# Kernel tuning notes

Hardware: AMD Instinct MI355X
Metric: run time of the kernel (lower is better)

The kernel has to match this reference:

```python
import jax, jax.numpy as jnp
import numpy as np
import math

B, N_TOK, C, H = 8, 1024, 384, 6
K, S, P = 3, 2, 1
OUT_C, HID = 384, 4 * 384
EPS = 1e-5
NEG_INF = float('-inf')


def _build_conv_mask(num_token, k, s, p):
    """Replicates ConvAttentionMask (include_cls_token=True). Returns (mask[(N+2),(N+2)], idx[(W,k^2)] with -1 for padding)."""
    I = int(math.sqrt(num_token))
    ref = np.arange(num_token).reshape(I, I)
    ref = np.pad(ref, ((0, p), (0, p)), constant_values=-1)
    cent = np.arange(k // 2 - p, I - k // 2 + p, s)
    cc = np.stack(np.meshgrid(cent, cent, indexing='ij'), -1).reshape(-1, 1, 2)  # cartesian_prod order
    ke = np.arange(-(k // 2), k // 2 + 1)
    kc = np.stack(np.meshgrid(ke, ke, indexing='ij'), -1).reshape(1, -1, 2)
    coords = cc + kc  # (W, k^2, 2); negative coords wrap like torch fancy indexing -> hit -1 padding
    idx = ref[coords[..., 0], coords[..., 1]]  # (W, k^2)
    mask = np.full((num_token, num_token), NEG_INF, np.float32)
    for w in idx:
        v = w[w >= 0]
        mask[np.ix_(v, v)] = 1.0
    idx = idx + (idx >= 0).astype(np.int32)  # shift for cls token; -1 stays -1
    mask = np.pad(mask, ((1, 0), (1, 0)), constant_values=1.0)  # cls row/col
    mask = np.pad(mask, ((0, 1), (0, 1)), constant_values=0.0)  # extra zero-padded token
    return mask, idx

MASK_NP, IDX_NP = _build_conv_mask(N_TOK, K, S, P)
W_WIN = IDX_NP.shape[0]
# torch negative index -1 on a length-(N_TOK+1) tensor -> wrap to last token
IDX_FLAT = np.where(IDX_NP < 0, IDX_NP + N_TOK + 1, IDX_NP).reshape(-1)


def _ln(x, w, b):
    mu = jnp.mean(x, -1, keepdims=True)
    var = jnp.mean(jnp.square(x - mu), -1, keepdims=True)
    return (x - mu) * jax.lax.rsqrt(var + EPS) * w + b


def setup_inputs() -> dict:
    key = jax.random.key(0)
    ks = jax.random.split(key, 8)
    sd = 0.02
    return {
        'x': jax.random.normal(ks[0], (B, N_TOK + 1, C), jnp.float32),
        'norm1_w': jnp.ones((C,), jnp.float32), 'norm1_b': jnp.zeros((C,), jnp.float32),
        'qkv_w': sd * jax.random.normal(ks[1], (3 * C, C), jnp.float32),
        'proj_w': sd * jax.random.normal(ks[2], (C, C), jnp.float32),
        'proj_b': jnp.zeros((C,), jnp.float32),
        'norm2_w': jnp.ones((C,), jnp.float32), 'norm2_b': jnp.zeros((C,), jnp.float32),
        'pool_w': sd * jax.random.normal(ks[3], (C, K * K * C), jnp.float32),
        'pool_b': jnp.zeros((C,), jnp.float32),
        'norm3_w': jnp.ones((C,), jnp.float32), 'norm3_b': jnp.zeros((C,), jnp.float32),
        'fc1_w': sd * jax.random.normal(ks[4], (HID, C), jnp.float32),
        'fc1_b': jnp.zeros((HID,), jnp.float32),
        'fc2_w': sd * jax.random.normal(ks[5], (OUT_C, HID), jnp.float32),
        'fc2_b': jnp.zeros((OUT_C,), jnp.float32),
    }


def reference(x, norm1_w, norm1_b, qkv_w, proj_w, proj_b, norm2_w, norm2_b,
              pool_w, pool_b, norm3_w, norm3_b, fc1_w, fc1_b, fc2_w, fc2_b):
    mask = jnp.asarray(MASK_NP)  # (N_TOK+2, N_TOK+2), values in {-inf, 0, 1}
    Bv, N, Cv = x.shape
    d = Cv // H
    h = _ln(x, norm1_w, norm1_b)
    h = jnp.pad(h, ((0, 0), (0, 1), (0, 0)))  # append zero token -> (B, N+1, C)
    M = N + 1
    # attention (scale = num_heads**-0.5 as in the source, qkv has no bias)
    qkv = (h @ qkv_w.T).reshape(Bv, M, 3, H, d).transpose(2, 0, 3, 1, 4)
    q, k, v = qkv[0], qkv[1], qkv[2]
    scores = jnp.einsum('bhqd,bhkd->bhqk', q, k) * (H ** -0.5)
    # multiplicative mask {-inf,0,1}: keep where 1, zero where 0, -inf where -inf (intended semantics)
    scores = jnp.where(mask == 1.0, scores, jnp.where(mask == 0.0, 0.0, NEG_INF))
    probs = jax.nn.softmax(scores, axis=-1)
    attn = jnp.einsum('bhqk,bhkd->bhqd', probs, v).transpose(0, 2, 1, 3).reshape(Bv, M, Cv)
    attn = attn @ proj_w.T + proj_b
    h = h + attn
    h = h[:, :-1, :]  # drop padded token -> (B, N, C)
    h = _ln(h, norm2_w, norm2_b)
    # conv-style pooling: gather k^2 tokens per window, project
    gathered = h[:, IDX_FLAT, :].reshape(Bv, W_WIN, K * K * Cv)
    tok = gathered @ pool_w.T + pool_b  # (B, W, C)
    h = jnp.concatenate([h[:, :1, :], tok], axis=1)  # prepend cls -> (B, W+1, C)
    h = _ln(h, norm3_w, norm3_b)
    h = jax.nn.gelu(h @ fc1_w.T + fc1_b, approximate=False)
    return h @ fc2_w.T + fc2_b  # (B, W+1, OUT_C)
```

## Files before the change

### kernel.cpp

```cpp
#include <hip/hip_runtime.h>


typedef unsigned short u16;
typedef unsigned int u32;
typedef short s16x8 __attribute__((ext_vector_type(8)));
typedef float f32x4 __attribute__((ext_vector_type(4)));

__device__ __forceinline__ float b2f(u16 u) {
    return __uint_as_float(((u32)u) << 16);
}
__device__ __forceinline__ u16 f2b(float f) {
    u32 u = __float_as_uint(f);
    return (u16)((u + 0x7FFFu + ((u >> 16) & 1u)) >> 16);
}
__device__ __forceinline__ void gload16(const void* g, void* l) {
    __builtin_amdgcn_global_load_lds(
        (const __attribute__((address_space(1))) void*)g,
        (__attribute__((address_space(3))) void*)l, 16, 0, 0);
}
__device__ __forceinline__ float wave_sum(float v) {
#pragma unroll
    for (int o = 32; o > 0; o >>= 1) v += __shfl_xor(v, o, 64);
    return v;
}
__device__ __forceinline__ float wave_max(float v) {
#pragma unroll
    for (int o = 32; o > 0; o >>= 1) v = fmaxf(v, __shfl_xor(v, o, 64));
    return v;
}
__device__ __forceinline__ float half_sum(float v) {
#pragma unroll
    for (int o = 16; o > 0; o >>= 1) v += __shfl_xor(v, o, 64);
    return v;
}
__device__ __forceinline__ float half_max(float v) {
#pragma unroll
    for (int o = 16; o > 0; o >>= 1) v = fmaxf(v, __shfl_xor(v, o, 64));
    return v;
}
__device__ __forceinline__ float dot8(const float* qsh, int d0, uint4 u) {
    return qsh[d0 + 0] * b2f((u16)(u.x)) + qsh[d0 + 1] * b2f((u16)(u.x >> 16)) +
           qsh[d0 + 2] * b2f((u16)(u.y)) + qsh[d0 + 3] * b2f((u16)(u.y >> 16)) +
           qsh[d0 + 4] * b2f((u16)(u.z)) + qsh[d0 + 5] * b2f((u16)(u.z >> 16)) +
           qsh[d0 + 6] * b2f((u16)(u.w)) + qsh[d0 + 7] * b2f((u16)(u.w >> 16));
}

#define CCH 384
#define SCALE 0.40824829046386302f
#define NEG_BIG (-1e30f)

#define W_QKV 0
#define W_PROJ 442368
#define W_POOL 589824
#define W_FC1 1916928
#define W_FC2 2506752
#define W_TOTAL 3096576

__device__ __forceinline__ void ln_from_f32(const float* in, const float* w,
                                            const float* bb, u16* out,
                                            int lane) {
    float v[6];
    float s = 0.f, ss = 0.f;
#pragma unroll
    for (int i = 0; i < 6; i++) {
        v[i] = in[lane + 64 * i];
        s += v[i];
        ss += v[i] * v[i];
    }
    s = wave_sum(s);
    ss = wave_sum(ss);
    float mu = s * (1.f / 384.f);
    float var = ss * (1.f / 384.f) - mu * mu;
    float inv = rsqrtf(var + 1e-5f);
#pragma unroll
    for (int i = 0; i < 6; i++) {
        int c = lane + 64 * i;
        out[c] = f2b((v[i] - mu) * inv * w[c] + bb[c]);
    }
}
__device__ __forceinline__ void ln_from_b16(const u16* in, const float* w,
                                            const float* bb, u16* out,
                                            int lane) {
    float v[6];
    float s = 0.f, ss = 0.f;
#pragma unroll
    for (int i = 0; i < 6; i++) {
        v[i] = b2f(in[lane + 64 * i]);
        s += v[i];
        ss += v[i] * v[i];
    }
    s = wave_sum(s);
    ss = wave_sum(ss);
    float mu = s * (1.f / 384.f);
    float var = ss * (1.f / 384.f) - mu * mu;
    float inv = rsqrtf(var + 1e-5f);
#pragma unroll
    for (int i = 0; i < 6; i++) {
        int c = lane + 64 * i;
        out[c] = f2b((v[i] - mu) * inv * w[c] + bb[c]);
    }
}

#define PRO_LN 2052
#define PRO_CVT 1512
#define PRO_ZERO 771
__global__ __launch_bounds__(256) void prologue(
    const float* __restrict__ x, const float* __restrict__ n1w,
    const float* __restrict__ n1b, u16* __restrict__ h1,
    const float* __restrict__ qkv_w, const float* __restrict__ proj_w,
    const float* __restrict__ pool_w, const float* __restrict__ fc1_w,
    const float* __restrict__ fc2_w, u16* __restrict__ wb,
    float* __restrict__ dout) {
    int bid = blockIdx.x, tid = threadIdx.x;
    if (bid < PRO_LN) {
        int wv = tid >> 6, lane = tid & 63;
        int row = bid * 4 + wv;
        int t = row % 1026, b = row / 1026;
        u16* out = h1 + (size_t)row * CCH;
        if (t == 1025) {
#pragma unroll
            for (int i = 0; i < 6; i++) out[lane + 64 * i] = 0;
            return;
        }
        ln_from_f32(x + ((size_t)b * 1025 + t) * CCH, n1w, n1b, out, lane);
    } else if (bid < PRO_LN + PRO_CVT) {
        size_t off = ((size_t)(bid - PRO_LN) * 256 + tid) * 8;
        if (off >= W_TOTAL) return;
        const float* src;
        size_t base;
        if (off < W_PROJ)       { src = qkv_w;  base = W_QKV; }
        else if (off < W_POOL)  { src = proj_w; base = W_PROJ; }
        else if (off < W_FC1)   { src = pool_w; base = W_POOL; }
        else if (off < W_FC2)   { src = fc1_w;  base = W_FC1; }
        else                    { src = fc2_w;  base = W_FC2; }
        size_t rel = off - base;
        float4 a = *(const float4*)(src + rel);
        float4 b = *(const float4*)(src + rel + 4);
        uint4 o;
        o.x = (u32)f2b(a.x) | ((u32)f2b(a.y) << 16);
        o.y = (u32)f2b(a.z) | ((u32)f2b(a.w) << 16);
        o.z = (u32)f2b(b.x) | ((u32)f2b(b.y) << 16);
        o.w = (u32)f2b(b.z) | ((u32)f2b(b.w) << 16);
        *(uint4*)(wb + off) = o;
    } else {
        size_t idx = ((size_t)(bid - PRO_LN - PRO_CVT) * 256 + tid) * 4;
        *(float4*)(dout + idx) = make_float4(0.f, 0.f, 0.f, 0.f);
    }
}

#define MID_LN 2050
#define MID_ZERO 768
__global__ __launch_bounds__(256) void midk(u16* __restrict__ h,
                                            const float* __restrict__ n2w,
                                            const float* __restrict__ n2b,
                                            float* __restrict__ tokf) {
    int bid = blockIdx.x, tid = threadIdx.x;
    if (bid < MID_LN) {
        int wv = tid >> 6, lane = tid & 63;
        int row = bid * 4 + wv;
        int b = row / 1025, t = row % 1025;
        u16* p = h + ((size_t)b * 1026 + t) * CCH;
        ln_from_b16(p, n2w, n2b, p, lane);
    } else {
        size_t idx = ((size_t)(bid - MID_LN) * 256 + tid) * 4;
        *(float4*)(tokf + idx) = make_float4(0.f, 0.f, 0.f, 0.f);
    }
}

__global__ __launch_bounds__(256) void ln3_concat(const u16* __restrict__ h2,
                                                  const float* __restrict__ tokf,
                                                  const float* __restrict__ w,
                                                  const float* __restrict__ bb,
                                                  u16* __restrict__ h3) {
    int tid = threadIdx.x;
    int wv = tid >> 6, lane = tid & 63;
    int row = blockIdx.x * 4 + wv;
    int b = row / 257, t = row % 257;
    u16* out = h3 + (size_t)row * CCH;
    if (t == 0) {
        ln_from_b16(h2 + (size_t)b * 1026 * CCH, w, bb, out, lane);
    } else {
        ln_from_f32(tokf + ((size_t)b * 256 + (t - 1)) * CCH, w, bb, out, lane);
    }
}

template <int TN, bool GATHER, int SPLITK, bool BIAS, bool GELU_ACT, bool RES,
          bool ATOMIC>
__global__ __launch_bounds__(256) void gemm_mf(const u16* __restrict__ A,
                                               int lda,
                                               const u16* __restrict__ Bwb,
                                               const float* __restrict__ bias,
                                               const u16* __restrict__ Res,
                                               void* __restrict__ Yv, int M,
                                               int N, int K) {
    __shared__ u16 Asl[128 * 32];
    __shared__ u16 Bsl[TN * 32];
    const int tid = threadIdx.x;
    const int wave = tid >> 6, lane = tid & 63;
    const int quad = lane >> 4, l15 = lane & 15;
    const int wvu = __builtin_amdgcn_readfirstlane(wave);
    const int m0 = blockIdx.y * 128, n0 = blockIdx.x * TN;
    const int kp = (SPLITK > 1) ? blockIdx.z : 0;
    const int KS = K / SPLITK;
    const int kbase = kp * KS;
    const int srow = tid >> 2;
    const int sseg = (tid & 3) ^ (srow & 3);

    f32x4 acc[2][TN / 16];
#pragma unroll
    for (int i = 0; i < 2; i++)
#pragma unroll
        for (int j = 0; j < TN / 16; j++) acc[i][j] = (f32x4){0.f, 0.f, 0.f, 0.f};

    for (int kt = 0; kt < KS; kt += 32) {
        const int kk = kbase + kt;
        const int kf = kk + sseg * 8;
#pragma unroll
        for (int L = 0; L < 2; L++) {
            int row = L * 64 + srow;
            const u16* src;
            if (GATHER) {
                int m = m0 + row;
                int b = m >> 8, w = m & 255;
                int j = kf / 384, rem = kf - j * 384;
                int pr = 2 * (w >> 4) + j / 3 - 1;
                int pc = 2 * (w & 15) + j % 3 - 1;
                int tok = (pr >= 0 && pr < 32 && pc >= 0 && pc < 32)
                              ? (32 * pr + pc + 1)
                              : 1024;
                src = A + ((size_t)b * 1026 + tok) * 384 + rem;
            } else {
                int m = m0 + row;
                if (m >= M) m = M - 1;
                src = A + (size_t)m * lda + kf;
            }
            gload16(src, &Asl[(size_t)(L * 256 + wvu * 64) * 8]);
        }
#pragma unroll
        for (int L = 0; L < TN / 64; L++) {
            int row = L * 64 + srow;
            gload16(Bwb + (size_t)(n0 + row) * K + kf,
                    &Bsl[(size_t)(L * 256 + wvu * 64) * 8]);
        }
        __syncthreads();
        s16x8 afr[2], bfr[TN / 16];
        const int rslot = (quad ^ (l15 & 3)) * 8;
#pragma unroll
        for (int ms = 0; ms < 2; ms++)
            afr[ms] =
                *(const s16x8*)(&Asl[(wave * 32 + ms * 16 + l15) * 32 + rslot]);
#pragma unroll
        for (int ns = 0; ns < TN / 16; ns++)
            bfr[ns] = *(const s16x8*)(&Bsl[(ns * 16 + l15) * 32 + rslot]);
#pragma unroll
        for (int ms = 0; ms < 2; ms++)
#pragma unroll
            for (int ns = 0; ns < TN / 16; ns++)
                acc[ms][ns] = __builtin_amdgcn_mfma_f32_16x16x32_bf16(
                    afr[ms], bfr[ns], acc[ms][ns], 0, 0, 0);
        __syncthreads();
    }
#pragma unroll
    for (int ms = 0; ms < 2; ms++) {
#pragma unroll
        for (int ns = 0; ns < TN / 16; ns++) {
            int n = n0 + ns * 16 + l15;
#pragma unroll
            for (int i = 0; i < 4; i++) {
                int m = m0 + wave * 32 + ms * 16 + quad * 4 + i;
                if (m >= M) continue;
                float v = acc[ms][ns][i];
                if (BIAS && (SPLITK == 1 || kp == 0)) v += bias[n];
                if (RES) v += b2f(Res[(size_t)m * N + n]);
                if (GELU_ACT) v = 0.5f * v * (1.f + erff(v * 0.70710678118f));
                if (ATOMIC)
                    atomicAdd((float*)Yv + (size_t)m * N + n, v);
                else
                    ((u16*)Yv)[(size_t)m * N + n] = f2b(v);
            }
        }
    }
}

__global__ __launch_bounds__(256) void attn_patch(u16* __restrict__ qkv) {
    __shared__ float qsh[4][2][64];
    int tid = threadIdx.x;
    int wv = tid >> 6, lane = tid & 63;
    int pair = blockIdx.x * 4 + wv;
    int idx = pair & 511;
    int hb = pair >> 9;
    int h = hb % 6, b = hb / 6;
    int hl = lane >> 5, l5 = lane & 31;
    int p0 = idx * 2;
    int p = p0 | hl;
    int r = p >> 5, c = p & 31;
    int rlo, rhi, clo, chi;
    if (r & 1) { rlo = (r - 2 < 0) ? 0 : r - 2; rhi = (r + 2 > 31) ? 31 : r + 2; }
    else       { rlo = (r - 1 < 0) ? 0 : r - 1; rhi = (r + 1 > 31) ? 31 : r + 1; }
    if (c & 1) { clo = (c - 2 < 0) ? 0 : c - 2; chi = (c + 2 > 31) ? 31 : c + 2; }
    else       { clo = (c - 1 < 0) ? 0 : c - 1; chi = (c + 1 > 31) ? 31 : c + 1; }
    int nr = rhi - rlo + 1, nc = chi - clo + 1;
    int nk = nr * nc + 1;
    int tok = 0;
    if (l5 >= 1 && l5 < nk) {
        int jj = l5 - 1;
        tok = 1 + ((rlo + jj / nc) << 5) + (clo + jj % nc);
    }
    u16* base = qkv + (size_t)b * 1026 * 1152 + h * 64;
    qsh[wv][0][lane] = b2f(base[(size_t)(1 + p0) * 1152 + lane]);
    qsh[wv][1][lane] = b2f(base[(size_t)(2 + p0) * 1152 + lane]);
    float sc = NEG_BIG;
    if (l5 < nk) {
        const u16* krow = base + (size_t)tok * 1152 + 384;
        float acc = 0.f;
#pragma unroll
        for (int d0 = 0; d0 < 64; d0 += 8)
            acc += dot8(qsh[wv][hl], d0, *(const uint4*)(krow + d0));
        sc = acc * SCALE;
    }
    float mx = fmaxf(half_max(sc), 0.f);
    float pe = (l5 < nk) ? expf(sc - mx) : 0.f;
    float Z = half_sum(pe) + expf(-mx);
    float o0 = 0.f, o1 = 0.f;
#pragma unroll
    for (int j = 0; j < 26; j++) {
        int t = __shfl(tok, (hl << 5) | j, 64);
        float wj = __shfl(pe, (hl << 5) | j, 64);
        u32 vv = *(const u32*)(base + (size_t)t * 1152 + 768 + 2 * l5);
        o0 += wj * b2f((u16)vv);
        o1 += wj * b2f((u16)(vv >> 16));
    }
    float zi = 1.f / Z;
    u32 packed = (u32)f2b(o0 * zi) | ((u32)f2b(o1 * zi) << 16);
    *(u32*)(base + (size_t)(1 + p) * 1152 + 2 * l5) = packed;
}

__global__ __launch_bounds__(1024) void attn_cls(u16* __restrict__ qkv) {
    int h = blockIdx.x % 6, b = blockIdx.x / 6;
    u16* base = qkv + (size_t)b * 1026 * 1152 + h * 64;
    int tid = threadIdx.x, lane = tid & 63, wv = tid >> 6;
    __shared__ float sc[1026];
    __shared__ float qsh[64];
    __shared__ float redmax[16], redsum[16];
    __shared__ float pv[16][64];
    if (tid < 64) qsh[tid] = b2f(base[tid]);
    __syncthreads();
    for (int key = tid; key < 1026; key += 1024) {
        const u16* krow = base + (size_t)key * 1152 + 384;
        float acc = 0.f;
#pragma unroll
        for (int d0 = 0; d0 < 64; d0 += 8)
            acc += dot8(qsh, d0, *(const uint4*)(krow + d0));
        sc[key] = acc * SCALE;
    }
    __syncthreads();
    float lm = NEG_BIG;
    for (int key = tid; key < 1026; key += 1024) lm = fmaxf(lm, sc[key]);
    lm = wave_max(lm);
    if (lane == 0) redmax[wv] = lm;
    __syncthreads();
    float mx = NEG_BIG;
#pragma unroll
    for (int i = 0; i < 16; i++) mx = fmaxf(mx, redmax[i]);
    float lsum = 0.f;
    for (int key = tid; key < 1026; key += 1024) {
        float e = expf(sc[key] - mx);
        sc[key] = e;
        lsum += e;
    }
    lsum = wave_sum(lsum);
    if (lane == 0) redsum[wv] = lsum;
    __syncthreads();
    float Z = 0.f;
#pragma unroll
    for (int i = 0; i < 16; i++) Z += redsum[i];
    float acc = 0.f;
#pragma unroll
    for (int t = 0; t < 65; t++) {
        int key = wv + 16 * t;
        bool ok = key < 1026;
        int kc = ok ? key : 1025;
        float p = ok ? sc[kc] : 0.f;
        acc += p * b2f(base[(size_t)kc * 1152 + 768 + lane]);
    }
    pv[wv][lane] = acc;
    __syncthreads();
    if (tid < 64) {
        float s = 0.f;
#pragma unroll
        for (int w2 = 0; w2 < 16; w2++) s += pv[w2][tid];
        base[tid] = f2b(s / Z);
        base[(size_t)1025 * 1152 + tid] = 0;
    }
}

extern "C" void kernel_launch(void* const* d_in, const int* in_sizes, int n_in,
                              void* d_out, int out_size, void* d_ws,
                              size_t ws_size, hipStream_t stream) {
    const float* x      = (const float*)d_in[0];
    const float* n1w    = (const float*)d_in[1];
    const float* n1b    = (const float*)d_in[2];
    const float* qkv_w  = (const float*)d_in[3];
    const float* proj_w = (const float*)d_in[4];
    const float* proj_b = (const float*)d_in[5];
    const float* n2w    = (const float*)d_in[6];
    const float* n2b    = (const float*)d_in[7];
    const float* pool_w = (const float*)d_in[8];
    const float* pool_b = (const float*)d_in[9];
    const float* n3w    = (const float*)d_in[10];
    const float* n3b    = (const float*)d_in[11];
    const float* fc1_w  = (const float*)d_in[12];
    const float* fc1_b  = (const float*)d_in[13];
    const float* fc2_w  = (const float*)d_in[14];
    const float* fc2_b  = (const float*)d_in[15];

    u16* ws = (u16*)d_ws;
    u16* h1    = ws;
    u16* qkvb  = ws + 3151872;
    u16* wb    = ws + 12607488;
    float* tokf = (float*)qkvb;
    u16* h3    = qkvb + 1572864;
    u16* mlp1  = qkvb + 2362368;

    prologue<<<PRO_LN + PRO_CVT + PRO_ZERO, 256, 0, stream>>>(
        x, n1w, n1b, h1, qkv_w, proj_w, pool_w, fc1_w, fc2_w, wb,
        (float*)d_out);
    gemm_mf<128, false, 1, false, false, false, false>
        <<<dim3(1152 / 128, 65), 256, 0, stream>>>(h1, 384, wb + W_QKV,
                                                   nullptr, nullptr, qkvb,
                                                   8208, 1152, 384);
    attn_patch<<<8 * 6 * 512 / 4, 256, 0, stream>>>(qkvb);
    attn_cls<<<8 * 6, 1024, 0, stream>>>(qkvb);
    gemm_mf<64, false, 1, true, false, true, false>
        <<<dim3(384 / 64, 65), 256, 0, stream>>>(qkvb, 1152, wb + W_PROJ,
                                                 proj_b, h1, h1, 8208, 384,
                                                 384);
    midk<<<MID_LN + MID_ZERO, 256, 0, stream>>>(h1, n2w, n2b, tokf);
    gemm_mf<64, true, 4, true, false, false, true>
        <<<dim3(384 / 64, 16, 4), 256, 0, stream>>>(h1, 384, wb + W_POOL,
                                                    pool_b, nullptr, tokf,
                                                    2048, 384, 3456);
    ln3_concat<<<8 * 257 / 4, 256, 0, stream>>>(h1, tokf, n3w, n3b, h3);
    gemm_mf<64, false, 1, true, true, false, false>
        <<<dim3(1536 / 64, 17), 256, 0, stream>>>(h3, 384, wb + W_FC1, fc1_b,
                                                  nullptr, mlp1, 2056, 1536,
                                                  384);
    gemm_mf<64, false, 4, true, false, false, true>
        <<<dim3(384 / 64, 17, 4), 256, 0, stream>>>(mlp1, 1536, wb + W_FC2,
                                                    fc2_b, nullptr, d_out,
                                                    2056, 384, 1536);
}
```

Measured before the change: 265.5 us.

## Stage shared K/V window tile in LDS for patch attention blocks

Each block of four query pairs (eight adjacent patch tokens in one row) now cooperatively loads the union of their 5x11 neighbourhood K and V rows, plus the cls token, into swizzled LDS using direct global-to-LDS loads. The score and PV loops then read from LDS instead of issuing scattered global loads per lane. This removes redundant global reads of overlapping neighbours across queries, at the cost of 16KB LDS per block and a block-wide barrier. Out-of-range slots point at the padding token.

Result: no change. 269.8 us (+1.6%).

```diff
diff --git a/kernel.cpp b/kernel.cpp
--- a/kernel.cpp
+++ b/kernel.cpp
@@ -283,17 +283,50 @@
 }
 
 __global__ __launch_bounds__(256) void attn_patch(u16* __restrict__ qkv) {
+    __shared__ u16 Ksh[64 * 64];
+    __shared__ u16 Vsh[64 * 64];
     __shared__ float qsh[4][2][64];
     int tid = threadIdx.x;
     int wv = tid >> 6, lane = tid & 63;
-    int pair = blockIdx.x * 4 + wv;
-    int idx = pair & 511;
-    int hb = pair >> 9;
+    int pair0 = blockIdx.x * 4;
+    int idx0 = pair0 & 511;
+    int hb = pair0 >> 9;
     int h = hb % 6, b = hb / 6;
+    int r = idx0 >> 4;
+    int c0 = (idx0 & 15) * 2;
+    u16* base = qkv + (size_t)b * 1026 * 1152 + h * 64;
+
+    int p0 = (idx0 + wv) * 2;
+    qsh[wv][0][lane] = b2f(base[(size_t)(1 + p0) * 1152 + lane]);
+    qsh[wv][1][lane] = b2f(base[(size_t)(2 + p0) * 1152 + lane]);
+
+#pragma unroll
+    for (int i = 0; i < 4; i++) {
+        int chunk = wv * 4 + i;
+        int isV = chunk >> 3;
+        int slot = (chunk & 7) * 8 + (lane >> 3);
+        int seg = lane & 7;
+        int tok;
+        if (slot < 55) {
+            int sr = slot / 11, sc2 = slot - sr * 11;
+            int kr = r - 2 + sr, kc = c0 - 1 + sc2;
+            tok = (kr >= 0 && kr < 32 && kc >= 0 && kc < 32)
+                      ? (1 + (kr << 5) + kc)
+                      : 1025;
+        } else {
+            tok = (slot == 55) ? 0 : 1025;
+        }
+        int sseg = seg ^ (slot & 7);
+        const u16* src =
+            base + (size_t)tok * 1152 + (isV ? 768 : 384) + sseg * 8;
+        u16* dst = (isV ? Vsh : Ksh) + (size_t)(chunk & 7) * 512;
+        gload16(src, dst);
+    }
+    __syncthreads();
+
     int hl = lane >> 5, l5 = lane & 31;
-    int p0 = idx * 2;
     int p = p0 | hl;
-    int r = p >> 5, c = p & 31;
+    int c = p & 31;
     int rlo, rhi, clo, chi;
     if (r & 1) { rlo = (r - 2 < 0) ? 0 : r - 2; rhi = (r + 2 > 31) ? 31 : r + 2; }
     else       { rlo = (r - 1 < 0) ? 0 : r - 1; rhi = (r + 1 > 31) ? 31 : r + 1; }
@@ -301,21 +334,22 @@
     else       { clo = (c - 1 < 0) ? 0 : c - 1; chi = (c + 1 > 31) ? 31 : c + 1; }
     int nr = rhi - rlo + 1, nc = chi - clo + 1;
     int nk = nr * nc + 1;
-    int tok = 0;
-    if (l5 >= 1 && l5 < nk) {
+    int slot = 56;
+    if (l5 == 0) slot = 55;
+    else if (l5 < nk) {
         int jj = l5 - 1;
-        tok = 1 + ((rlo + jj / nc) << 5) + (clo + jj % nc);
-    }
-    u16* base = qkv + (size_t)b * 1026 * 1152 + h * 64;
-    qsh[wv][0][lane] = b2f(base[(size_t)(1 + p0) * 1152 + lane]);
-    qsh[wv][1][lane] = b2f(base[(size_t)(2 + p0) * 1152 + lane]);
+        int kr = rlo + jj / nc, kc = clo + jj % nc;
+        slot = (kr - (r - 2)) * 11 + (kc - (c0 - 1));
+    }
     float sc = NEG_BIG;
     if (l5 < nk) {
-        const u16* krow = base + (size_t)tok * 1152 + 384;
+        const u16* krow = Ksh + slot * 64;
+        int sw = slot & 7;
         float acc = 0.f;
 #pragma unroll
-        for (int d0 = 0; d0 < 64; d0 += 8)
-            acc += dot8(qsh[wv][hl], d0, *(const uint4*)(krow + d0));
+        for (int d0 = 0; d0 < 8; d0++)
+            acc += dot8(qsh[wv][hl], d0 * 8,
+                        *(const uint4*)(krow + (d0 ^ sw) * 8));
         sc = acc * SCALE;
     }
     float mx = fmaxf(half_max(sc), 0.f);
@@ -324,9 +358,11 @@
     float o0 = 0.f, o1 = 0.f;
 #pragma unroll
     for (int j = 0; j < 26; j++) {
-        int t = __shfl(tok, (hl << 5) | j, 64);
+        int ts = __shfl(slot, (hl << 5) | j, 64);
         float wj = __shfl(pe, (hl << 5) | j, 64);
-        u32 vv = *(const u32*)(base + (size_t)t * 1152 + 768 + 2 * l5);
+        const u16* vrow = Vsh + ts * 64;
+        int g = (l5 >> 2) ^ (ts & 7);
+        u32 vv = *(const u32*)(vrow + g * 8 + (l5 & 3) * 2);
         o0 += wj * b2f((u16)vv);
         o1 += wj * b2f((u16)(vv >> 16));
     }
```
